# Kernel tuning notes

Hardware: AMD Instinct MI355X
Metric: run time of the kernel (lower is better)

Reference implementation:

```python
import jax, jax.numpy as jnp
import numpy as np
from jax import lax

N = 2048
BS = 64
NUM_ITR = 25


def setup_inputs() -> dict:
    key = jax.random.key(0)
    k1, k2, k3, k4, k5 = jax.random.split(key, 5)
    scale = 0.5 / np.sqrt(N)  # keep iteration matrices contractive so the recurrence stays bounded
    H = jax.random.normal(k1, (N, N), dtype=jnp.float32) / np.sqrt(N)
    Dinv = jax.random.normal(k2, (N, N), dtype=jnp.float32) * scale
    U = jax.random.normal(k3, (N, N), dtype=jnp.float32) * scale
    invM = jax.random.normal(k4, (N, N), dtype=jnp.float32) * scale
    y = jax.random.normal(k5, (BS, N), dtype=jnp.float32)
    return {"num_itr": NUM_ITR, "bs": BS, "y": y, "H": H, "Dinv": Dinv, "U": U, "invM": invM}


def reference(num_itr, bs, y, H, Dinv, U, invM):
    n = H.shape[0]
    s0 = jnp.zeros((bs, n), dtype=y.dtype)
    yMF = y @ H.T                 # [bs, n]
    s_init = yMF @ Dinv           # initial Gauss-Seidel estimate

    def step(s, _):
        s_next = (yMF - s @ U) @ invM
        return s_next, s_next

    s_final, traj_iters = lax.scan(step, s_init, None, length=num_itr)
    # traj matches the torch list: [zeros, s_1, ..., s_num_itr]
    traj = jnp.concatenate([s0[None], traj_iters], axis=0)  # [num_itr+1, bs, n]
    return s_final, traj
```

## Files before the change

### kernel.cpp

```cpp
#include <hip/hip_runtime.h>
#include <hip/hip_bf16.h>

#define NDIM 2048
#define BS   64
#define NM4  (NDIM * NDIM / 4)
#define BSN  ((size_t)BS * NDIM)
#define SMEM_BYTES 69632

typedef __bf16 bf16_t;
typedef __bf16 bf16x4 __attribute__((ext_vector_type(4)));
typedef __bf16 bf16x8 __attribute__((ext_vector_type(8)));
typedef float  f32x4  __attribute__((ext_vector_type(4)));

__global__ __launch_bounds__(256) void prep(
    const float* __restrict__ H, const float* __restrict__ U,
    const float* __restrict__ Dinv, const float* __restrict__ invM,
    const float* __restrict__ y,
    bf16_t* __restrict__ H16, bf16_t* __restrict__ U16,
    bf16_t* __restrict__ Dt, bf16_t* __restrict__ iMt,
    bf16_t* __restrict__ y16, float* __restrict__ traj0) {
  __shared__ bf16_t tile[32][33];
  int b = blockIdx.x, tid = threadIdx.x;
  if (b < 8192) {
    int idx = b * 256 + tid;
    const float* src = (idx < NM4) ? H : U;
    bf16_t* dst = (idx < NM4) ? H16 : U16;
    int i = (idx < NM4) ? idx : idx - NM4;
    float4 v = ((const float4*)src)[i];
    bf16x4 o = {(bf16_t)v.x, (bf16_t)v.y, (bf16_t)v.z, (bf16_t)v.w};
    ((bf16x4*)dst)[i] = o;
    if (idx < BS * NDIM / 4) {
      float4 w = ((const float4*)y)[idx];
      bf16x4 o2 = {(bf16_t)w.x, (bf16_t)w.y, (bf16_t)w.z, (bf16_t)w.w};
      ((bf16x4*)y16)[idx] = o2;
      ((float4*)traj0)[idx] = make_float4(0.f, 0.f, 0.f, 0.f);
    }
  } else {
    int id = b - 8192;
    int bx = id & 63, by = id >> 6;
    int tx = tid & 31, ty = tid >> 5;
    const float* src[2] = {Dinv, invM};
    bf16_t* dst[2] = {Dt, iMt};
#pragma unroll
    for (int m = 0; m < 2; ++m) {
      __syncthreads();
#pragma unroll
      for (int i = 0; i < 4; ++i)
        tile[ty + i * 8][tx] =
            (bf16_t)src[m][(size_t)(by * 32 + ty + i * 8) * NDIM + bx * 32 + tx];
      __syncthreads();
#pragma unroll
      for (int i = 0; i < 4; ++i)
        dst[m][(size_t)(bx * 32 + ty + i * 8) * NDIM + by * 32 + tx] = tile[tx][ty + i * 8];
    }
  }
}

__device__ __forceinline__ void wgemm_role(
    const bf16_t* __restrict__ A, const bf16_t* __restrict__ Bt,
    bf16_t* __restrict__ C, int blk, char* smem) {
  bf16x8* As_lo = (bf16x8*)smem;
  bf16x8* Bs_lo = (bf16x8*)(smem + 8192);
  bf16x8* As_hi = (bf16x8*)(smem + 16384);
  bf16x8* Bs_hi = (bf16x8*)(smem + 24576);
  int tid = threadIdx.x, lane = tid & 63, wave = tid >> 6;
  int kh = wave >> 2, wq = wave & 3;
  int m0 = (blk >> 4) * 128, n0 = (blk & 15) * 128;
  int wr16 = (wq >> 1) * 4, wc16 = (wq & 1) * 4;
  int ml = lane & 15, q = lane >> 4;

  f32x4 acc[4][4];
#pragma unroll
  for (int i = 0; i < 4; ++i)
#pragma unroll
    for (int j = 0; j < 4; ++j) acc[i][j] = (f32x4){0.f, 0.f, 0.f, 0.f};

  int sg = tid >> 6, sln = tid & 63;
  int srow = sg * 16 + (sln & 15), skq = (sln >> 4) << 3;

  for (int k0 = 0; k0 < 1024; k0 += 32) {
    __syncthreads();
    As_lo[tid] = *(const bf16x8*)(A  + (size_t)(m0 + srow) * NDIM + k0 + skq);
    Bs_lo[tid] = *(const bf16x8*)(Bt + (size_t)(n0 + srow) * NDIM + k0 + skq);
    As_hi[tid] = *(const bf16x8*)(A  + (size_t)(m0 + srow) * NDIM + 1024 + k0 + skq);
    Bs_hi[tid] = *(const bf16x8*)(Bt + (size_t)(n0 + srow) * NDIM + 1024 + k0 + skq);
    __syncthreads();
    bf16x8* Asb = kh ? As_hi : As_lo;
    bf16x8* Bsb = kh ? Bs_hi : Bs_lo;
    bf16x8 af[4], bfr[4];
#pragma unroll
    for (int i = 0; i < 4; ++i) {
      af[i]  = Asb[(wr16 + i) * 64 + lane];
      bfr[i] = Bsb[(wc16 + i) * 64 + lane];
    }
#pragma unroll
    for (int i = 0; i < 4; ++i)
#pragma unroll
      for (int j = 0; j < 4; ++j)
        acc[i][j] = __builtin_amdgcn_mfma_f32_16x16x32_bf16(af[i], bfr[j], acc[i][j], 0, 0, 0);
  }

  f32x4* exch = (f32x4*)smem;
  __syncthreads();
  if (kh == 1) {
#pragma unroll
    for (int f = 0; f < 16; ++f)
      exch[(f * 4 + wq) * 64 + lane] = acc[f >> 2][f & 3];
  }
  __syncthreads();
  if (kh == 0) {
    int wr = wr16 * 16, wc = wc16 * 16;
#pragma unroll
    for (int i = 0; i < 4; ++i)
#pragma unroll
      for (int j = 0; j < 4; ++j) {
        f32x4 s = acc[i][j] + exch[((i * 4 + j) * 4 + wq) * 64 + lane];
#pragma unroll
        for (int r = 0; r < 4; ++r)
          C[(size_t)(m0 + wr + i * 16 + q * 4 + r) * NDIM + n0 + wc + j * 16 + ml] =
              (bf16_t)s[r];
      }
  }
}

__device__ __forceinline__ void skinny_role(
    const bf16_t* __restrict__ A, const bf16_t* __restrict__ Bt, int n0, char* smem,
    const float* __restrict__ add, float sign,
    float* o32, float* o32b, bf16_t* o16) {
  bf16x8* panel = (bf16x8*)smem;
  f32x4* red = (f32x4*)(smem + 65536);
  int tid = threadIdx.x, lane = tid & 63, wave = tid >> 6;
#pragma unroll
  for (int i = 0; i < 8; ++i) {
    int F = i * 512 + tid, c = F >> 6, ln = F & 63;
    panel[F] = *(const bf16x8*)(Bt + (size_t)(n0 + (ln & 15)) * NDIM + c * 32 + ((ln >> 4) << 3));
  }
  __syncthreads();

  int ms = (wave & 3) * 16, kh = wave >> 2;
  int ml = lane & 15, q = lane >> 4;
  const bf16x8* Ap = (const bf16x8*)(A + (size_t)(ms + ml) * NDIM) + q + kh * 128;
  const bf16x8* Bp = panel + lane + kh * 2048;

  f32x4 acc[4];
  acc[0] = acc[1] = acc[2] = acc[3] = (f32x4){0.f, 0.f, 0.f, 0.f};
#pragma unroll
  for (int c = 0; c < 32; ++c) {
    bf16x8 a = Ap[c * 4];
    bf16x8 b = Bp[c * 64];
    acc[c & 3] = __builtin_amdgcn_mfma_f32_16x16x32_bf16(a, b, acc[c & 3], 0, 0, 0);
  }
  f32x4 s = (acc[0] + acc[1]) + (acc[2] + acc[3]);

  if (wave >= 4) red[(wave & 3) * 64 + lane] = s;
  __syncthreads();
  if (wave < 4) {
    s += red[wave * 64 + lane];
    int mrow = ms + q * 4, col = n0 + ml;
#pragma unroll
    for (int r = 0; r < 4; ++r) {
      size_t o = (size_t)(mrow + r) * NDIM + col;
      float v = sign * s[r];
      if (add) v += add[o];
      if (o32)  o32[o]  = v;
      if (o32b) o32b[o] = v;
      if (o16)  o16[o]  = (bf16_t)v;
    }
  }
}

__device__ __forceinline__ void transpose_role(const bf16_t* __restrict__ src,
                                               bf16_t* __restrict__ dst, int blk, char* smem) {
  bf16_t (*tile)[72] = (bf16_t(*)[72])smem;
  int tid = threadIdx.x;
  int bx = blk & 31, by = blk >> 5;
  {
    int r = tid >> 3, c8 = (tid & 7) * 8;
    *(bf16x8*)&tile[r][c8] = *(const bf16x8*)(src + (size_t)(by * 64 + r) * NDIM + bx * 64 + c8);
  }
  __syncthreads();
  {
    int r = tid >> 3, c8 = (tid & 7) * 8;
    bf16x8 o;
#pragma unroll
    for (int j = 0; j < 8; ++j) o[j] = tile[c8 + j][r];
    *(bf16x8*)(dst + (size_t)(bx * 64 + r) * NDIM + by * 64 + c8) = o;
  }
}

__global__ __launch_bounds__(512, 2) void megaA(
    const bf16_t* __restrict__ U16, const bf16_t* __restrict__ iMt16,
    const bf16_t* __restrict__ y16, const bf16_t* __restrict__ H16,
    bf16_t* __restrict__ Wrm, bf16_t* __restrict__ yMF16) {
  __shared__ char smem[SMEM_BYTES];
  int b = blockIdx.x;
  if (b < 256) wgemm_role(U16, iMt16, Wrm, b, smem);
  else         skinny_role(y16, H16, (b - 256) * 16, smem, nullptr, 1.f, nullptr, nullptr, yMF16);
}

__global__ __launch_bounds__(512, 2) void megaB(
    const bf16_t* __restrict__ Wrm, const bf16_t* __restrict__ yMF16,
    const bf16_t* __restrict__ iMt16, const bf16_t* __restrict__ Dt16,
    bf16_t* __restrict__ Wt, float* __restrict__ c32, bf16_t* __restrict__ c16,
    bf16_t* __restrict__ z0) {
  __shared__ char smem[SMEM_BYTES];
  int b = blockIdx.x;
  if (b < 1024)      transpose_role(Wrm, Wt, b, smem);
  else if (b < 1152) skinny_role(yMF16, iMt16, (b - 1024) * 16, smem, nullptr, 1.f, c32, nullptr, c16);
  else               skinny_role(yMF16, Dt16, (b - 1152) * 16, smem, nullptr, 1.f, nullptr, nullptr, z0);
}

__global__ __launch_bounds__(512, 2) void megaC(
    const bf16_t* __restrict__ Wt, const bf16_t* __restrict__ Wrm,
    const bf16_t* __restrict__ z0, const bf16_t* __restrict__ c16,
    const float* __restrict__ c32,
    bf16_t* __restrict__ W2t, float* __restrict__ traj1, bf16_t* __restrict__ z0b,
    float* __restrict__ c2_32, bf16_t* __restrict__ c2_16) {
  __shared__ char smem[SMEM_BYTES];
  int b = blockIdx.x;
  if (b < 256)      wgemm_role(Wt, Wrm, W2t, b, smem);
  else if (b < 384) skinny_role(z0, Wt, (b - 256) * 16, smem, c32, -1.f, traj1, nullptr, z0b);
  else              skinny_role(c16, Wt, (b - 384) * 16, smem, c32, -1.f, c2_32, nullptr, c2_16);
}

__global__ __launch_bounds__(512, 2) void megaD(
    const bf16_t* __restrict__ W2t, const bf16_t* __restrict__ z0,
    const bf16_t* __restrict__ c2_16, const float* __restrict__ c2_32,
    bf16_t* __restrict__ W2rm, float* __restrict__ traj2, float* __restrict__ traj3,
    bf16_t* __restrict__ zA, float* __restrict__ c4_32) {
  __shared__ char smem[SMEM_BYTES];
  int b = blockIdx.x;
  if (b < 1024)      transpose_role(W2t, W2rm, b, smem);
  else if (b < 1152) skinny_role(z0, W2t, (b - 1024) * 16, smem, c2_32, 1.f, traj2, nullptr, zA);
  else if (b < 1280) skinny_role(z0 + BSN, W2t, (b - 1152) * 16, smem, c2_32, 1.f, traj3, nullptr, zA + BSN);
  else               skinny_role(c2_16, W2t, (b - 1280) * 16, smem, c2_32, 1.f, c4_32, nullptr, nullptr);
}

__global__ __launch_bounds__(512, 2) void megaE(
    const bf16_t* __restrict__ W2t, const bf16_t* __restrict__ W2rm,
    const bf16_t* __restrict__ zA_in, const float* __restrict__ c2_32,
    bf16_t* __restrict__ W4t, float* __restrict__ traj4, float* __restrict__ traj5,
    bf16_t* __restrict__ zA) {
  __shared__ char smem[SMEM_BYTES];
  int b = blockIdx.x;
  if (b < 256)      wgemm_role(W2t, W2rm, W4t, b, smem);
  else if (b < 384) skinny_role(zA_in, W2t, (b - 256) * 16, smem, c2_32, 1.f, traj4, nullptr, zA + 2 * BSN);
  else              skinny_role(zA_in + BSN, W2t, (b - 384) * 16, smem, c2_32, 1.f, traj5, nullptr, zA + 3 * BSN);
}

__global__ __launch_bounds__(512, 2) void quad_step(
    const bf16_t* __restrict__ zin, const bf16_t* __restrict__ W4t,
    const float* __restrict__ c4_32, float* __restrict__ trajb,
    bf16_t* __restrict__ zout, float* __restrict__ sfin) {
  __shared__ char smem[SMEM_BYTES];
  int b = blockIdx.x, ci = b & 3, p = b >> 2;
  skinny_role(zin + (size_t)ci * BSN, W4t, p * 16, smem, c4_32, 1.f,
              trajb + (size_t)ci * BSN, (ci == 3) ? sfin : nullptr,
              zout + (size_t)ci * BSN);
}

extern "C" void kernel_launch(void* const* d_in, const int* in_sizes, int n_in,
                              void* d_out, int out_size, void* d_ws, size_t ws_size,
                              hipStream_t stream) {
  const float* y    = (const float*)d_in[2];
  const float* H    = (const float*)d_in[3];
  const float* Dinv = (const float*)d_in[4];
  const float* U    = (const float*)d_in[5];
  const float* invM = (const float*)d_in[6];

  float* out     = (float*)d_out;
  float* s_final = out;
  float* traj    = out + BSN;

  char* ws = (char*)d_ws;
  size_t off = 0;
  auto alloc = [&](size_t bytes) -> void* {
    void* p = ws + off;
    off += (bytes + 255) & ~(size_t)255;
    return p;
  };
  bf16_t* U16   = (bf16_t*)alloc((size_t)NDIM * NDIM * 2);
  bf16_t* Dt16  = (bf16_t*)alloc((size_t)NDIM * NDIM * 2);
  bf16_t* iMt16 = (bf16_t*)alloc((size_t)NDIM * NDIM * 2);
  bf16_t* H16   = (bf16_t*)alloc((size_t)NDIM * NDIM * 2);
  bf16_t* Wrm   = (bf16_t*)alloc((size_t)NDIM * NDIM * 2);
  bf16_t* Wt    = (bf16_t*)alloc((size_t)NDIM * NDIM * 2);
  bf16_t* y16   = (bf16_t*)alloc(BSN * 2);
  bf16_t* yMF16 = (bf16_t*)alloc(BSN * 2);
  bf16_t* c16   = (bf16_t*)alloc(BSN * 2);
  bf16_t* c2_16 = (bf16_t*)alloc(BSN * 2);
  float*  c32   = (float*)alloc(BSN * 4);
  float*  c2_32 = (float*)alloc(BSN * 4);
  float*  c4_32 = (float*)alloc(BSN * 4);
  bf16_t* z0    = (bf16_t*)alloc(2 * BSN * 2);
  bf16_t* zA    = (bf16_t*)alloc(4 * BSN * 2);
  bf16_t* zB    = (bf16_t*)alloc(4 * BSN * 2);
  bf16_t* W2t   = H16;
  bf16_t* W2rm  = U16;
  bf16_t* W4t   = Dt16;

  prep<<<12288, 256, 0, stream>>>(H, U, Dinv, invM, y, H16, U16, Dt16, iMt16, y16, traj);
  megaA<<<384, 512, 0, stream>>>(U16, iMt16, y16, H16, Wrm, yMF16);
  megaB<<<1280, 512, 0, stream>>>(Wrm, yMF16, iMt16, Dt16, Wt, c32, c16, z0);
  megaC<<<512, 512, 0, stream>>>(Wt, Wrm, z0, c16, c32, W2t, traj + BSN, z0 + BSN, c2_32, c2_16);
  megaD<<<1408, 512, 0, stream>>>(W2t, z0, c2_16, c2_32, W2rm, traj + 2 * BSN, traj + 3 * BSN,
                                  zA, c4_32);
  megaE<<<512, 512, 0, stream>>>(W2t, W2rm, zA, c2_32, W4t, traj + 4 * BSN, traj + 5 * BSN, zA);

  bf16_t* zcur = zA;
  bf16_t* znxt = zB;
  for (int g = 0; g < 5; ++g) {
    float* sfin = (g == 4) ? s_final : nullptr;
    quad_step<<<512, 512, 0, stream>>>(zcur, W4t, c4_32, traj + (size_t)(6 + 4 * g) * BSN,
                                       znxt, sfin);
    bf16_t* tmp = zcur; zcur = znxt; znxt = tmp;
  }
}
```

Measured before the change: 419.8 us.

## Pipeline wide GEMM with async global-to-LDS loads and restructure prep kernels

The square GEMM role now uses direct global-to-LDS loads with a 4-stage ring buffer and explicit vmcnt waits, dropping the split-K reduction in favor of a 2x4 tile per wave. The skinny role also loads its panel through async LDS loads and uses 8 accumulators for more MFMA ILP. Prep is restructured to 512 threads with 64x64 transpose tiles, and launch bounds are raised to 4 blocks per CU. The aim is to hide global latency and cut barrier overhead, at the cost of register pressure from the raised occupancy target and reliance on inline asm waitcnt ordering.

```diff
diff --git a/kernel.cpp b/kernel.cpp
--- a/kernel.cpp
+++ b/kernel.cpp
@@ -12,151 +12,166 @@
 typedef __bf16 bf16x8 __attribute__((ext_vector_type(8)));
 typedef float  f32x4  __attribute__((ext_vector_type(4)));
 
-__global__ __launch_bounds__(256) void prep(
+__device__ __forceinline__ void gload16(const void* g, void* lds) {
+  __builtin_amdgcn_global_load_lds(
+      (const __attribute__((address_space(1))) void*)g,
+      (__attribute__((address_space(3))) void*)lds, 16, 0, 0);
+}
+
+#define WB4 asm volatile("s_waitcnt vmcnt(4)\n\ts_barrier" ::: "memory")
+#define WB2 asm volatile("s_waitcnt vmcnt(2)\n\ts_barrier" ::: "memory")
+#define WB0 asm volatile("s_waitcnt vmcnt(0)\n\ts_barrier" ::: "memory")
+
+__global__ __launch_bounds__(512) void prep(
     const float* __restrict__ H, const float* __restrict__ U,
     const float* __restrict__ Dinv, const float* __restrict__ invM,
     const float* __restrict__ y,
     bf16_t* __restrict__ H16, bf16_t* __restrict__ U16,
     bf16_t* __restrict__ Dt, bf16_t* __restrict__ iMt,
     bf16_t* __restrict__ y16, float* __restrict__ traj0) {
-  __shared__ bf16_t tile[32][33];
+  __shared__ bf16_t tile[64][72];
   int b = blockIdx.x, tid = threadIdx.x;
-  if (b < 8192) {
-    int idx = b * 256 + tid;
-    const float* src = (idx < NM4) ? H : U;
-    bf16_t* dst = (idx < NM4) ? H16 : U16;
-    int i = (idx < NM4) ? idx : idx - NM4;
-    float4 v = ((const float4*)src)[i];
-    bf16x4 o = {(bf16_t)v.x, (bf16_t)v.y, (bf16_t)v.z, (bf16_t)v.w};
-    ((bf16x4*)dst)[i] = o;
-    if (idx < BS * NDIM / 4) {
-      float4 w = ((const float4*)y)[idx];
+  if (b < 1024) {
+#pragma unroll
+    for (int i = 0; i < 4; ++i) {
+      int idx = b * 2048 + i * 512 + tid;
+      const float* src = (idx < NM4) ? H : U;
+      bf16_t* dst = (idx < NM4) ? H16 : U16;
+      int j = (idx < NM4) ? idx : idx - NM4;
+      float4 v = ((const float4*)src)[j];
+      bf16x4 o = {(bf16_t)v.x, (bf16_t)v.y, (bf16_t)v.z, (bf16_t)v.w};
+      ((bf16x4*)dst)[j] = o;
+    }
+    int yi = b * 512 + tid;
+    if (yi < BS * NDIM / 4) {
+      float4 w = ((const float4*)y)[yi];
       bf16x4 o2 = {(bf16_t)w.x, (bf16_t)w.y, (bf16_t)w.z, (bf16_t)w.w};
-      ((bf16x4*)y16)[idx] = o2;
-      ((float4*)traj0)[idx] = make_float4(0.f, 0.f, 0.f, 0.f);
+      ((bf16x4*)y16)[yi] = o2;
+      ((float4*)traj0)[yi] = make_float4(0.f, 0.f, 0.f, 0.f);
     }
   } else {
-    int id = b - 8192;
-    int bx = id & 63, by = id >> 6;
-    int tx = tid & 31, ty = tid >> 5;
-    const float* src[2] = {Dinv, invM};
-    bf16_t* dst[2] = {Dt, iMt};
-#pragma unroll
-    for (int m = 0; m < 2; ++m) {
-      __syncthreads();
-#pragma unroll
-      for (int i = 0; i < 4; ++i)
-        tile[ty + i * 8][tx] =
-            (bf16_t)src[m][(size_t)(by * 32 + ty + i * 8) * NDIM + bx * 32 + tx];
-      __syncthreads();
-#pragma unroll
-      for (int i = 0; i < 4; ++i)
-        dst[m][(size_t)(bx * 32 + ty + i * 8) * NDIM + by * 32 + tx] = tile[tx][ty + i * 8];
-    }
+    int id = b - 1024;
+    const float* src = (id < 1024) ? Dinv : invM;
+    bf16_t* dst = (id < 1024) ? Dt : iMt;
+    id &= 1023;
+    int bx = id & 31, by = id >> 5;
+    int r = tid >> 3, c8 = (tid & 7) * 8;
+    const float* sp = src + (size_t)(by * 64 + r) * NDIM + bx * 64 + c8;
+    float4 v0 = *(const float4*)sp;
+    float4 v1 = *(const float4*)(sp + 4);
+    bf16_t* t = &tile[r][c8];
+    t[0] = (bf16_t)v0.x; t[1] = (bf16_t)v0.y; t[2] = (bf16_t)v0.z; t[3] = (bf16_t)v0.w;
+    t[4] = (bf16_t)v1.x; t[5] = (bf16_t)v1.y; t[6] = (bf16_t)v1.z; t[7] = (bf16_t)v1.w;
+    __syncthreads();
+    bf16x8 o;
+#pragma unroll
+    for (int j = 0; j < 8; ++j) o[j] = tile[c8 + j][r];
+    *(bf16x8*)(dst + (size_t)(bx * 64 + r) * NDIM + by * 64 + c8) = o;
   }
 }
 
 __device__ __forceinline__ void wgemm_role(
     const bf16_t* __restrict__ A, const bf16_t* __restrict__ Bt,
     bf16_t* __restrict__ C, int blk, char* smem) {
-  bf16x8* As_lo = (bf16x8*)smem;
-  bf16x8* Bs_lo = (bf16x8*)(smem + 8192);
-  bf16x8* As_hi = (bf16x8*)(smem + 16384);
-  bf16x8* Bs_hi = (bf16x8*)(smem + 24576);
   int tid = threadIdx.x, lane = tid & 63, wave = tid >> 6;
-  int kh = wave >> 2, wq = wave & 3;
   int m0 = (blk >> 4) * 128, n0 = (blk & 15) * 128;
-  int wr16 = (wq >> 1) * 4, wc16 = (wq & 1) * 4;
-  int ml = lane & 15, q = lane >> 4;
-
-  f32x4 acc[4][4];
-#pragma unroll
-  for (int i = 0; i < 4; ++i)
+  int rl = lane & 15, q = lane >> 4;
+  const bf16_t* Ag = A  + (size_t)(m0 + wave * 16 + rl) * NDIM + q * 8;
+  const bf16_t* Bg = Bt + (size_t)(n0 + wave * 16 + rl) * NDIM + q * 8;
+  char* ldsA = smem + wave * 1024;
+  char* ldsB = smem + 8192 + wave * 1024;
+
+  f32x4 acc[2][4];
+#pragma unroll
+  for (int i = 0; i < 2; ++i)
 #pragma unroll
     for (int j = 0; j < 4; ++j) acc[i][j] = (f32x4){0.f, 0.f, 0.f, 0.f};
 
-  int sg = tid >> 6, sln = tid & 63;
-  int srow = sg * 16 + (sln & 15), skq = (sln >> 4) << 3;
-
-  for (int k0 = 0; k0 < 1024; k0 += 32) {
-    __syncthreads();
-    As_lo[tid] = *(const bf16x8*)(A  + (size_t)(m0 + srow) * NDIM + k0 + skq);
-    Bs_lo[tid] = *(const bf16x8*)(Bt + (size_t)(n0 + srow) * NDIM + k0 + skq);
-    As_hi[tid] = *(const bf16x8*)(A  + (size_t)(m0 + srow) * NDIM + 1024 + k0 + skq);
-    Bs_hi[tid] = *(const bf16x8*)(Bt + (size_t)(n0 + srow) * NDIM + 1024 + k0 + skq);
-    __syncthreads();
-    bf16x8* Asb = kh ? As_hi : As_lo;
-    bf16x8* Bsb = kh ? Bs_hi : Bs_lo;
-    bf16x8 af[4], bfr[4];
-#pragma unroll
-    for (int i = 0; i < 4; ++i) {
-      af[i]  = Asb[(wr16 + i) * 64 + lane];
-      bfr[i] = Bsb[(wc16 + i) * 64 + lane];
-    }
-#pragma unroll
-    for (int i = 0; i < 4; ++i)
-#pragma unroll
-      for (int j = 0; j < 4; ++j)
-        acc[i][j] = __builtin_amdgcn_mfma_f32_16x16x32_bf16(af[i], bfr[j], acc[i][j], 0, 0, 0);
-  }
-
-  f32x4* exch = (f32x4*)smem;
-  __syncthreads();
-  if (kh == 1) {
-#pragma unroll
-    for (int f = 0; f < 16; ++f)
-      exch[(f * 4 + wq) * 64 + lane] = acc[f >> 2][f & 3];
-  }
-  __syncthreads();
-  if (kh == 0) {
-    int wr = wr16 * 16, wc = wc16 * 16;
-#pragma unroll
-    for (int i = 0; i < 4; ++i)
-#pragma unroll
-      for (int j = 0; j < 4; ++j) {
-        f32x4 s = acc[i][j] + exch[((i * 4 + j) * 4 + wq) * 64 + lane];
-#pragma unroll
-        for (int r = 0; r < 4; ++r)
-          C[(size_t)(m0 + wr + i * 16 + q * 4 + r) * NDIM + n0 + wc + j * 16 + ml] =
-              (bf16_t)s[r];
-      }
-  }
+  int wr2 = (wave & 3) * 2, wc4 = (wave >> 2) * 4;
+
+#define STAGE(s)                                  \
+  {                                               \
+    int _b = (s) & 3, _k = (s) * 32;              \
+    gload16(Ag + _k, ldsA + _b * 16384);          \
+    gload16(Bg + _k, ldsB + _b * 16384);          \
+  }
+#define COMPUTE(bb)                                                            \
+  {                                                                            \
+    bf16x8* As = (bf16x8*)(smem + (bb) * 16384);                               \
+    bf16x8* Bs = (bf16x8*)(smem + (bb) * 16384 + 8192);                        \
+    bf16x8 af0 = As[wr2 * 64 + lane];                                          \
+    bf16x8 af1 = As[(wr2 + 1) * 64 + lane];                                    \
+    bf16x8 bf0 = Bs[wc4 * 64 + lane];                                          \
+    bf16x8 bf1 = Bs[(wc4 + 1) * 64 + lane];                                    \
+    bf16x8 bf2 = Bs[(wc4 + 2) * 64 + lane];                                    \
+    bf16x8 bf3 = Bs[(wc4 + 3) * 64 + lane];                                    \
+    acc[0][0] = __builtin_amdgcn_mfma_f32_16x16x32_bf16(af0, bf0, acc[0][0], 0, 0, 0); \
+    acc[0][1] = __builtin_amdgcn_mfma_f32_16x16x32_bf16(af0, bf1, acc[0][1], 0, 0, 0); \
+    acc[0][2] = __builtin_amdgcn_mfma_f32_16x16x32_bf16(af0, bf2, acc[0][2], 0, 0, 0); \
+    acc[0][3] = __builtin_amdgcn_mfma_f32_16x16x32_bf16(af0, bf3, acc[0][3], 0, 0, 0); \
+    acc[1][0] = __builtin_amdgcn_mfma_f32_16x16x32_bf16(af1, bf0, acc[1][0], 0, 0, 0); \
+    acc[1][1] = __builtin_amdgcn_mfma_f32_16x16x32_bf16(af1, bf1, acc[1][1], 0, 0, 0); \
+    acc[1][2] = __builtin_amdgcn_mfma_f32_16x16x32_bf16(af1, bf2, acc[1][2], 0, 0, 0); \
+    acc[1][3] = __builtin_amdgcn_mfma_f32_16x16x32_bf16(af1, bf3, acc[1][3], 0, 0, 0); \
+  }
+
+  STAGE(0); STAGE(1); STAGE(2);
+  int s = 3;
+#pragma unroll 1
+  for (int k = 0; k < 60; k += 4) {
+    WB4; STAGE(s); ++s; COMPUTE(0);
+    WB4; STAGE(s); ++s; COMPUTE(1);
+    WB4; STAGE(s); ++s; COMPUTE(2);
+    WB4; STAGE(s); ++s; COMPUTE(3);
+  }
+  WB4; STAGE(63); COMPUTE(0);
+  WB4; COMPUTE(1);
+  WB2; COMPUTE(2);
+  WB0; COMPUTE(3);
+#undef STAGE
+#undef COMPUTE
+
+#pragma unroll
+  for (int i = 0; i < 2; ++i)
+#pragma unroll
+    for (int j = 0; j < 4; ++j)
+#pragma unroll
+      for (int r = 0; r < 4; ++r)
+        C[(size_t)(m0 + (wr2 + i) * 16 + q * 4 + r) * NDIM + n0 + (wc4 + j) * 16 + rl] =
+            (bf16_t)acc[i][j][r];
 }
 
 __device__ __forceinline__ void skinny_role(
     const bf16_t* __restrict__ A, const bf16_t* __restrict__ Bt, int n0, char* smem,
     const float* __restrict__ add, float sign,
     float* o32, float* o32b, bf16_t* o16) {
-  bf16x8* panel = (bf16x8*)smem;
+  int tid = threadIdx.x, lane = tid & 63, wave = tid >> 6;
+  int rl = lane & 15, q = lane >> 4;
+#pragma unroll
+  for (int i = 0; i < 8; ++i) {
+    const bf16_t* g = Bt + (size_t)(n0 + rl) * NDIM + (i * 8 + wave) * 32 + q * 8;
+    gload16(g, smem + (size_t)(i * 512 + wave * 64) * 16);
+  }
+  __syncthreads();
+
+  int ms = (wave & 3) * 16, kh = wave >> 2;
+  const bf16x8* Ap = (const bf16x8*)(A + (size_t)(ms + rl) * NDIM) + q + kh * 128;
+  const bf16x8* Bp = (const bf16x8*)smem + lane + kh * 2048;
+
+  f32x4 acc[8];
+#pragma unroll
+  for (int i = 0; i < 8; ++i) acc[i] = (f32x4){0.f, 0.f, 0.f, 0.f};
+#pragma unroll
+  for (int c = 0; c < 32; ++c)
+    acc[c & 7] = __builtin_amdgcn_mfma_f32_16x16x32_bf16(Ap[c * 4], Bp[c * 64], acc[c & 7], 0, 0, 0);
+  f32x4 s = ((acc[0] + acc[1]) + (acc[2] + acc[3])) + ((acc[4] + acc[5]) + (acc[6] + acc[7]));
+
   f32x4* red = (f32x4*)(smem + 65536);
-  int tid = threadIdx.x, lane = tid & 63, wave = tid >> 6;
-#pragma unroll
-  for (int i = 0; i < 8; ++i) {
-    int F = i * 512 + tid, c = F >> 6, ln = F & 63;
-    panel[F] = *(const bf16x8*)(Bt + (size_t)(n0 + (ln & 15)) * NDIM + c * 32 + ((ln >> 4) << 3));
-  }
-  __syncthreads();
-
-  int ms = (wave & 3) * 16, kh = wave >> 2;
-  int ml = lane & 15, q = lane >> 4;
-  const bf16x8* Ap = (const bf16x8*)(A + (size_t)(ms + ml) * NDIM) + q + kh * 128;
-  const bf16x8* Bp = panel + lane + kh * 2048;
-
-  f32x4 acc[4];
-  acc[0] = acc[1] = acc[2] = acc[3] = (f32x4){0.f, 0.f, 0.f, 0.f};
-#pragma unroll
-  for (int c = 0; c < 32; ++c) {
-    bf16x8 a = Ap[c * 4];
-    bf16x8 b = Bp[c * 64];
-    acc[c & 3] = __builtin_amdgcn_mfma_f32_16x16x32_bf16(a, b, acc[c & 3], 0, 0, 0);
-  }
-  f32x4 s = (acc[0] + acc[1]) + (acc[2] + acc[3]);
-
   if (wave >= 4) red[(wave & 3) * 64 + lane] = s;
   __syncthreads();
   if (wave < 4) {
     s += red[wave * 64 + lane];
-    int mrow = ms + q * 4, col = n0 + ml;
+    int mrow = ms + q * 4, col = n0 + rl;
 #pragma unroll
     for (int r = 0; r < 4; ++r) {
       size_t o = (size_t)(mrow + r) * NDIM + col;
@@ -174,21 +189,16 @@
   bf16_t (*tile)[72] = (bf16_t(*)[72])smem;
   int tid = threadIdx.x;
   int bx = blk & 31, by = blk >> 5;
-  {
-    int r = tid >> 3, c8 = (tid & 7) * 8;
-    *(bf16x8*)&tile[r][c8] = *(const bf16x8*)(src + (size_t)(by * 64 + r) * NDIM + bx * 64 + c8);
-  }
+  int r = tid >> 3, c8 = (tid & 7) * 8;
+  *(bf16x8*)&tile[r][c8] = *(const bf16x8*)(src + (size_t)(by * 64 + r) * NDIM + bx * 64 + c8);
   __syncthreads();
-  {
-    int r = tid >> 3, c8 = (tid & 7) * 8;
-    bf16x8 o;
-#pragma unroll
-    for (int j = 0; j < 8; ++j) o[j] = tile[c8 + j][r];
-    *(bf16x8*)(dst + (size_t)(bx * 64 + r) * NDIM + by * 64 + c8) = o;
-  }
-}
-
-__global__ __launch_bounds__(512, 2) void megaA(
+  bf16x8 o;
+#pragma unroll
+  for (int j = 0; j < 8; ++j) o[j] = tile[c8 + j][r];
+  *(bf16x8*)(dst + (size_t)(bx * 64 + r) * NDIM + by * 64 + c8) = o;
+}
+
+__global__ __launch_bounds__(512, 4) void megaA(
     const bf16_t* __restrict__ U16, const bf16_t* __restrict__ iMt16,
     const bf16_t* __restrict__ y16, const bf16_t* __restrict__ H16,
     bf16_t* __restrict__ Wrm, bf16_t* __restrict__ yMF16) {
@@ -198,7 +208,7 @@
   else         skinny_role(y16, H16, (b - 256) * 16, smem, nullptr, 1.f, nullptr, nullptr, yMF16);
 }
 
-__global__ __launch_bounds__(512, 2) void megaB(
+__global__ __launch_bounds__(512, 4) void megaB(
     const bf16_t* __restrict__ Wrm, const bf16_t* __restrict__ yMF16,
     const bf16_t* __restrict__ iMt16, const bf16_t* __restrict__ Dt16,
     bf16_t* __restrict__ Wt, float* __restrict__ c32, bf16_t* __restrict__ c16,
@@ -210,7 +220,7 @@
   else               skinny_role(yMF16, Dt16, (b - 1152) * 16, smem, nullptr, 1.f, nullptr, nullptr, z0);
 }
 
-__global__ __launch_bounds__(512, 2) void megaC(
+__global__ __launch_bounds__(512, 4) void megaC(
     const bf16_t* __restrict__ Wt, const bf16_t* __restrict__ Wrm,
     const bf16_t* __restrict__ z0, const bf16_t* __restrict__ c16,
     const float* __restrict__ c32,
@@ -223,7 +233,7 @@
   else              skinny_role(c16, Wt, (b - 384) * 16, smem, c32, -1.f, c2_32, nullptr, c2_16);
 }
 
-__global__ __launch_bounds__(512, 2) void megaD(
+__global__ __launch_bounds__(512, 4) void megaD(
     const bf16_t* __restrict__ W2t, const bf16_t* __restrict__ z0,
     const bf16_t* __restrict__ c2_16, const float* __restrict__ c2_32,
     bf16_t* __restrict__ W2rm, float* __restrict__ traj2, float* __restrict__ traj3,
@@ -236,7 +246,7 @@
   else               skinny_role(c2_16, W2t, (b - 1280) * 16, smem, c2_32, 1.f, c4_32, nullptr, nullptr);
 }
 
-__global__ __launch_bounds__(512, 2) void megaE(
+__global__ __launch_bounds__(512, 4) void megaE(
     const bf16_t* __restrict__ W2t, const bf16_t* __restrict__ W2rm,
     const bf16_t* __restrict__ zA_in, const float* __restrict__ c2_32,
     bf16_t* __restrict__ W4t, float* __restrict__ traj4, float* __restrict__ traj5,
@@ -248,7 +258,7 @@
   else              skinny_role(zA_in + BSN, W2t, (b - 384) * 16, smem, c2_32, 1.f, traj5, nullptr, zA + 3 * BSN);
 }
 
-__global__ __launch_bounds__(512, 2) void quad_step(
+__global__ __launch_bounds__(512, 4) void quad_step(
     const bf16_t* __restrict__ zin, const bf16_t* __restrict__ W4t,
     const float* __restrict__ c4_32, float* __restrict__ trajb,
     bf16_t* __restrict__ zout, float* __restrict__ sfin) {
@@ -299,7 +309,7 @@
   bf16_t* W2rm  = U16;
   bf16_t* W4t   = Dt16;
 
-  prep<<<12288, 256, 0, stream>>>(H, U, Dinv, invM, y, H16, U16, Dt16, iMt16, y16, traj);
+  prep<<<3072, 512, 0, stream>>>(H, U, Dinv, invM, y, H16, U16, Dt16, iMt16, y16, traj);
   megaA<<<384, 512, 0, stream>>>(U16, iMt16, y16, H16, Wrm, yMF16);
   megaB<<<1280, 512, 0, stream>>>(Wrm, yMF16, iMt16, Dt16, Wt, c32, c16, z0);
   megaC<<<512, 512, 0, stream>>>(Wt, Wrm, z0, c16, c32, W2t, traj + BSN, z0 + BSN, c2_32, c2_16);
```

New measurement: 389.2 us. 1.08x faster.
